# Kernel optimization log

Measured on AMD Instinct MI355X. Metric: run time of the kernel, lower is better.

## Reference

```python
import jax, jax.numpy as jnp
import numpy as np

HIDDEN = 1024
HEADS = 16
HEAD_DIM = HIDDEN // HEADS
EPS = 1e-5


def setup_inputs() -> dict:
    key = jax.random.key(0)
    ks = jax.random.split(key, 9)
    B, S, H = 2, 2048, HIDDEN
    scale = 1.0 / np.sqrt(H)
    inp = {
        "hidden_states": jax.random.normal(ks[0], (B, S, H), dtype=jnp.float32),
        "Wq": jax.random.normal(ks[1], (H, H), dtype=jnp.float32) * scale,
        "bq": jnp.zeros((H,), jnp.float32),
        "Wk": jax.random.normal(ks[2], (H, H), dtype=jnp.float32) * scale,
        "bk": jnp.zeros((H,), jnp.float32),
        "Wv": jax.random.normal(ks[3], (H, H), dtype=jnp.float32) * scale,
        "bv": jnp.zeros((H,), jnp.float32),
        "Wo": jax.random.normal(ks[4], (H, H), dtype=jnp.float32) * scale,
        "bo": jnp.zeros((H,), jnp.float32),
        "gamma": jnp.ones((H,), jnp.float32),
        "beta": jnp.zeros((H,), jnp.float32),
    }
    return inp


def reference(hidden_states, Wq, bq, Wk, bk, Wv, bv, Wo, bo, gamma, beta):
    B, S, H = hidden_states.shape
    residual = hidden_states

    def shape(x):  # [B,S,H] -> [B,heads,S,head_dim]
        return x.reshape(B, S, HEADS, HEAD_DIM).transpose(0, 2, 1, 3)

    q = shape(hidden_states @ Wq + bq)
    k = shape(hidden_states @ Wk + bk)
    v = shape(hidden_states @ Wv + bv)

    scores = jnp.einsum("bhqd,bhkd->bhqk", q, k) / jnp.sqrt(
        jnp.asarray(HEAD_DIM, hidden_states.dtype))
    probs = jax.nn.softmax(scores, axis=-1)
    context = jnp.einsum("bhqk,bhkd->bhqd", probs, v)
    context = context.transpose(0, 2, 1, 3).reshape(B, S, H)

    output = context @ Wo + bo
    x = output + residual
    mu = jnp.mean(x, axis=-1, keepdims=True)
    var = jnp.mean(jnp.square(x - mu), axis=-1, keepdims=True)
    return (x - mu) * jax.lax.rsqrt(var + EPS) * gamma + beta
```

## Files before the change

kernel.cpp:

```cpp
#include <hip/hip_runtime.h>
#include <hip/hip_bf16.h>
#include <math.h>

#define HIDDEN 1024
#define HEADS 16
#define HEAD_DIM 64
#define EPS 1e-5f

typedef __attribute__((ext_vector_type(8))) short bf16x8;
typedef __attribute__((ext_vector_type(4))) float f32x4;

#if defined(__has_builtin)
#if __has_builtin(__builtin_amdgcn_exp2f)
#define EXP2(x) __builtin_amdgcn_exp2f(x)
#endif
#endif
#ifndef EXP2
#define EXP2(x) exp2f(x)
#endif

#define QSCALE 0.18033688011112042f

__device__ __forceinline__ short f2bf(float f) {
    union { float f; unsigned u; } v; v.f = f;
    unsigned r = v.u + 0x7fffu + ((v.u >> 16) & 1u);
    return (short)(r >> 16);
}

__device__ __forceinline__ void gl_lds16(const void* g, void* l) {
    __builtin_amdgcn_global_load_lds(
        (const __attribute__((address_space(1))) void*)g,
        (__attribute__((address_space(3))) void*)l, 16, 0, 0);
}

__global__ __launch_bounds__(256) void prep_kernel(
    const float* __restrict__ X,
    const float* __restrict__ Wq, const float* __restrict__ Wk,
    const float* __restrict__ Wv, const float* __restrict__ Wo,
    const float* __restrict__ bq, const float* __restrict__ bk,
    const float* __restrict__ bv,
    short* __restrict__ Xb, short* __restrict__ Wt3, short* __restrict__ Wot,
    float* __restrict__ b3)
{
    const int z = blockIdx.z;
    __shared__ short tile[32][33];
    if (z < 4) {
        const float* W = (z == 0) ? Wq : (z == 1) ? Wk : (z == 2) ? Wv : Wo;
        short* dst = (z < 3) ? (Wt3 + (size_t)z * 1024 * 1024) : Wot;
        const float scale = (z == 0) ? QSCALE : 1.0f;
        int n0 = blockIdx.x * 32, k0 = blockIdx.y * 32;
        int tx = threadIdx.x & 31, ty = threadIdx.x >> 5;
        #pragma unroll
        for (int i = 0; i < 32; i += 8)
            tile[ty + i][tx] = f2bf(W[(size_t)(k0 + ty + i) * 1024 + n0 + tx] * scale);
        __syncthreads();
        #pragma unroll
        for (int i = 0; i < 32; i += 8)
            dst[(size_t)(n0 + ty + i) * 1024 + k0 + tx] = tile[tx][ty + i];
    } else if (z < 8) {
        int l = (z - 4) * 1024 + blockIdx.y * 32 + blockIdx.x;
        int i = (l * 256 + threadIdx.x) * 4;
        float4 v = *(const float4*)(X + i);
        short o[4] = { f2bf(v.x), f2bf(v.y), f2bf(v.z), f2bf(v.w) };
        *(uint2*)(Xb + i) = *(uint2*)o;
    } else {
        int i = (blockIdx.y * 32 + blockIdx.x) * 256 + threadIdx.x;
        if (i < 3072) {
            float v = (i < 1024) ? bq[i] * QSCALE
                    : (i < 2048) ? bk[i - 1024] : bv[i - 2048];
            b3[i] = v;
        }
    }
}

template<int BM>
__global__ __launch_bounds__(256) void gemm_bt_mfma(
    const short* __restrict__ A, const short* __restrict__ Bt,
    const float* __restrict__ bias,
    void* __restrict__ C0, int ldc0,
    void* __restrict__ C1, int split_col, int ldc1,
    const float* __restrict__ resid,
    int M, int N, int K, int out_bf16)
{
    constexpr int MT = BM / 32;
    constexpr int ACH = BM / 32;
    __shared__ short As[2][BM * 64];
    __shared__ short Bs[2][128 * 64];
    const int tid = threadIdx.x;
    const int wave = tid >> 6, lane = tid & 63;
    const int ln16 = lane & 15, quad = lane >> 4;
    const int wm = (wave >> 1) * (BM / 2), wn = (wave & 1) * 64;

    const int gx = gridDim.x;
    int bid = blockIdx.y * gx + blockIdx.x;
    const int cpx = (gx * gridDim.y) >> 3;
    bid = (bid & 7) * cpx + (bid >> 3);
    const int brow = (bid / gx) * BM, bcol = (bid % gx) * 128;

    const int kr  = lane >> 3;
    const int kb8 = lane & 7;

    f32x4 acc[MT][4];
    #pragma unroll
    for (int mt = 0; mt < MT; ++mt)
        #pragma unroll
        for (int nt = 0; nt < 4; ++nt) acc[mt][nt] = (f32x4){0.f, 0.f, 0.f, 0.f};

    auto stage = [&](int p, int kt) {
        #pragma unroll
        for (int i = 0; i < ACH; ++i) {
            int ci = wave * ACH + i;
            int r  = ci * 8 + kr;
            int csrc = (kb8 ^ (r & 7)) * 8;
            gl_lds16(A + (size_t)(brow + r) * K + kt * 64 + csrc, &As[p][ci * 512]);
        }
        #pragma unroll
        for (int i = 0; i < 4; ++i) {
            int ci = wave * 4 + i;
            int r  = ci * 8 + kr;
            int csrc = (kb8 ^ (r & 7)) * 8;
            gl_lds16(Bt + (size_t)(bcol + r) * K + kt * 64 + csrc, &Bs[p][ci * 512]);
        }
    };

    const int NKT = K / 64;
    stage(0, 0);
    __syncthreads();

    for (int kt = 0; kt < NKT; ++kt) {
        const int cur = kt & 1;
        if (kt + 1 < NKT) stage(cur ^ 1, kt + 1);

        #pragma unroll
        for (int kk = 0; kk < 2; ++kk) {
            bf16x8 af[MT], bf[4];
            #pragma unroll
            for (int mt = 0; mt < MT; ++mt) {
                int r = wm + mt * 16 + ln16;
                af[mt] = *(const bf16x8*)&As[cur][r * 64 + (((kk * 4 + quad) ^ (r & 7)) * 8)];
            }
            #pragma unroll
            for (int nt = 0; nt < 4; ++nt) {
                int r = wn + nt * 16 + ln16;
                bf[nt] = *(const bf16x8*)&Bs[cur][r * 64 + (((kk * 4 + quad) ^ (r & 7)) * 8)];
            }
            #pragma unroll
            for (int mt = 0; mt < MT; ++mt)
                #pragma unroll
                for (int nt = 0; nt < 4; ++nt)
                    acc[mt][nt] = __builtin_amdgcn_mfma_f32_16x16x32_bf16(
                        af[mt], bf[nt], acc[mt][nt], 0, 0, 0);
        }
        __syncthreads();
    }

    void* Cp = C0; int ld = ldc0; int coff = 0;
    if (bcol >= split_col) { Cp = C1; ld = ldc1; coff = split_col; }

    #pragma unroll
    for (int mt = 0; mt < MT; ++mt) {
        #pragma unroll
        for (int r = 0; r < 4; ++r) {
            int row = brow + wm + mt * 16 + quad * 4 + r;
            #pragma unroll
            for (int nt = 0; nt < 4; ++nt) {
                int col = bcol + wn + nt * 16 + ln16;
                float v = acc[mt][nt][r] + bias[col];
                if (resid) v += resid[(size_t)row * N + col];
                if (out_bf16) ((short*)Cp)[(size_t)row * ld + (col - coff)] = f2bf(v);
                else          ((float*)Cp)[(size_t)row * ld + (col - coff)] = v;
            }
        }
    }
}

__global__ __launch_bounds__(256) void vtranspose_kernel(
    const short* __restrict__ Vb, short* __restrict__ VT)
{
    __shared__ short t[64][72];
    const int c0 = blockIdx.x * 64;
    const int r0 = blockIdx.y * 64;
    const int tid = threadIdx.x;
    #pragma unroll
    for (int i = 0; i < 2; ++i) {
        int idx = tid + i * 256;
        int r = idx >> 3, cc = (idx & 7) * 8;
        *(uint4*)&t[r][cc] = *(const uint4*)(Vb + (size_t)(r0 + r) * 1024 + c0 + cc);
    }
    __syncthreads();
    #pragma unroll
    for (int i = 0; i < 2; ++i) {
        int idx = tid + i * 256;
        int c = idx >> 3, rr = (idx & 7) * 8;
        short tmp[8];
        #pragma unroll
        for (int j = 0; j < 8; ++j) tmp[j] = t[rr + j][c];
        *(uint4*)(VT + (size_t)(c0 + c) * 4096 + r0 + rr) = *(uint4*)tmp;
    }
}

__global__ __launch_bounds__(256, 3) void attn_mfma_kernel(
    const short* __restrict__ QKb, const short* __restrict__ VT,
    short* __restrict__ Ctx)
{
    const int S = 2048;
    const int h = blockIdx.x, qt = blockIdx.y, b = blockIdx.z;
    const int tid = threadIdx.x;
    const int wave = tid >> 6, lane = tid & 63;
    const int ln16 = lane & 15, quad = lane >> 4;

    __shared__ alignas(16) char smem[49152];
    short* Ks = (short*)smem;
    short* Vs = (short*)(smem + 16384);
    char*  Pw = smem + 32768 + wave * 4096;

    bf16x8 qf[4][2];
    #pragma unroll
    for (int qg = 0; qg < 4; ++qg)
        #pragma unroll
        for (int kb = 0; kb < 2; ++kb)
            qf[qg][kb] = *(const bf16x8*)(QKb +
                (size_t)(b * S + qt * 64 + qg * 16 + ln16) * 2048 +
                h * 64 + kb * 32 + quad * 8);

    f32x4 of[4][4];
    float rs[4] = {0.f, 0.f, 0.f, 0.f};
    #pragma unroll
    for (int qg = 0; qg < 4; ++qg)
        #pragma unroll
        for (int nt = 0; nt < 4; ++nt) of[qg][nt] = (f32x4){0.f, 0.f, 0.f, 0.f};

    auto stage = [&](int kt) {
        const int kr  = lane >> 3;
        const int kb8 = lane & 7;
        const int vr  = lane >> 4;
        const int vb16 = lane & 15;
        #pragma unroll
        for (int i = 0; i < 4; ++i) {
            int r = wave * 32 + i * 8 + kr;
            int ksrc = (kb8 ^ (r & 7)) * 8;
            gl_lds16(QKb + (size_t)(b * S + kt * 128 + r) * 2048 + 1024 + h * 64 + ksrc,
                     Ks + (wave * 32 + i * 8) * 64);
            int d = wave * 16 + i * 4 + vr;
            int vsrc = (vb16 ^ (d & 15)) * 8;
            gl_lds16(VT + (size_t)(h * 64 + d) * 4096 + b * S + kt * 128 + vsrc,
                     Vs + (wave * 16 + i * 4) * 128);
        }
    };

    stage(0);
    __syncthreads();

    const int t0w = wave * 32;

    for (int kt = 0; kt < 16; ++kt) {
        bf16x8 kf[2][2], vf[4];
        #pragma unroll
        for (int kblk = 0; kblk < 2; ++kblk) {
            int rloc = t0w + kblk * 16 + ln16;
            kf[kblk][0] = *(const bf16x8*)&Ks[rloc * 64 + ((quad ^ (rloc & 7)) * 8)];
            kf[kblk][1] = *(const bf16x8*)&Ks[rloc * 64 + (((4 + quad) ^ (rloc & 7)) * 8)];
        }
        #pragma unroll
        for (int nt = 0; nt < 4; ++nt) {
            int d = nt * 16 + ln16;
            vf[nt] = *(const bf16x8*)&Vs[d * 128 + (((wave * 4 + quad) ^ (d & 15)) * 8)];
        }
        __syncthreads();
        if (kt + 1 < 16) stage(kt + 1);

        #pragma unroll
        for (int kblk = 0; kblk < 2; ++kblk) {
            f32x4 a[4];
            __builtin_amdgcn_s_setprio(1);
            #pragma unroll
            for (int qg = 0; qg < 4; ++qg) {
                a[qg] = (f32x4){0.f, 0.f, 0.f, 0.f};
                a[qg] = __builtin_amdgcn_mfma_f32_16x16x32_bf16(kf[kblk][0], qf[qg][0], a[qg], 0, 0, 0);
            }
            #pragma unroll
            for (int qg = 0; qg < 4; ++qg)
                a[qg] = __builtin_amdgcn_mfma_f32_16x16x32_bf16(kf[kblk][1], qf[qg][1], a[qg], 0, 0, 0);
            __builtin_amdgcn_s_setprio(0);
            #pragma unroll
            for (int qg = 0; qg < 4; ++qg) {
                float p0 = EXP2(a[qg][0]), p1 = EXP2(a[qg][1]);
                float p2 = EXP2(a[qg][2]), p3 = EXP2(a[qg][3]);
                rs[qg] += (p0 + p1) + (p2 + p3);
                union { __hip_bfloat162 h2; unsigned u; } c01, c23;
                c01.h2 = __float22bfloat162_rn(make_float2(p0, p1));
                c23.h2 = __float22bfloat162_rn(make_float2(p2, p3));
                uint2 w; w.x = c01.u; w.y = c23.u;
                int qrow = qg * 16 + ln16;
                int key = (qrow >> 1) & 3;
                int bblk = (kblk * 2 + (quad >> 1)) ^ key;
                *(uint2*)(Pw + qrow * 64 + bblk * 16 + (quad & 1) * 8) = w;
            }
        }

        bf16x8 pf[4];
        #pragma unroll
        for (int qg = 0; qg < 4; ++qg) {
            int qrow = qg * 16 + ln16;
            int key = (qrow >> 1) & 3;
            pf[qg] = *(const bf16x8*)(Pw + qrow * 64 + ((quad ^ key) * 16));
        }
        __builtin_amdgcn_s_setprio(1);
        #pragma unroll
        for (int nt = 0; nt < 4; ++nt)
            #pragma unroll
            for (int qg = 0; qg < 4; ++qg)
                of[qg][nt] = __builtin_amdgcn_mfma_f32_16x16x32_bf16(pf[qg], vf[nt], of[qg][nt], 0, 0, 0);
        __builtin_amdgcn_s_setprio(0);

        __syncthreads();
    }

    #pragma unroll
    for (int qg = 0; qg < 4; ++qg) {
        rs[qg] += __shfl_xor(rs[qg], 16, 64);
        rs[qg] += __shfl_xor(rs[qg], 32, 64);
    }

    float* Rw = (float*)(smem + wave * 4864);
    float* Lb = (float*)(smem + 4 * 4864);

    if (quad == 0) {
        #pragma unroll
        for (int qg = 0; qg < 4; ++qg)
            Lb[wave * 64 + qg * 16 + ln16] = rs[qg];
    }

    const int rq  = tid >> 2;
    const int rd0 = (tid & 3) * 4;
    float inv = 0.f;

    #pragma unroll
    for (int nt = 0; nt < 4; ++nt) {
        #pragma unroll
        for (int qg = 0; qg < 4; ++qg)
            #pragma unroll
            for (int r = 0; r < 4; ++r)
                Rw[(qg * 16 + quad * 4 + r) * 19 + ln16] = of[qg][nt][r];
        __syncthreads();
        if (nt == 0) {
            float l = Lb[rq] + Lb[64 + rq] + Lb[128 + rq] + Lb[192 + rq];
            inv = 1.f / l;
        }
        short o4[4];
        #pragma unroll
        for (int j = 0; j < 4; ++j) {
            int d = rd0 + j;
            float s = 0.f;
            #pragma unroll
            for (int w = 0; w < 4; ++w)
                s += ((const float*)(smem + w * 4864))[rq * 19 + d];
            o4[j] = f2bf(s * inv);
        }
        *(uint2*)(Ctx + (size_t)(b * S + qt * 64 + rq) * 1024 + h * 64 + nt * 16 + rd0) =
            *(uint2*)o4;
        __syncthreads();
    }
}

__global__ __launch_bounds__(256) void resln_kernel(
    const float* __restrict__ xin, const float* __restrict__ gamma,
    const float* __restrict__ beta, float* __restrict__ out)
{
    const int row = blockIdx.x;
    const int tid = threadIdx.x;
    const int wid = tid >> 6, lane = tid & 63;
    __shared__ float red[8];

    float4 x = *(const float4*)(xin + (size_t)row * HIDDEN + tid * 4);
    float s = x.x + x.y + x.z + x.w;
    #pragma unroll
    for (int off = 32; off > 0; off >>= 1) s += __shfl_xor(s, off, 64);
    if (lane == 0) red[wid] = s;
    __syncthreads();
    float mu = (red[0] + red[1] + red[2] + red[3]) * (1.f / HIDDEN);

    float dx = x.x - mu, dy = x.y - mu, dz = x.z - mu, dw = x.w - mu;
    float v = dx * dx + dy * dy + dz * dz + dw * dw;
    #pragma unroll
    for (int off = 32; off > 0; off >>= 1) v += __shfl_xor(v, off, 64);
    if (lane == 0) red[4 + wid] = v;
    __syncthreads();
    float var = (red[4] + red[5] + red[6] + red[7]) * (1.f / HIDDEN);
    float rstd = rsqrtf(var + EPS);

    float4 g = *(const float4*)(gamma + tid * 4);
    float4 bt = *(const float4*)(beta + tid * 4);
    float4 o;
    o.x = dx * rstd * g.x + bt.x;
    o.y = dy * rstd * g.y + bt.y;
    o.z = dz * rstd * g.z + bt.z;
    o.w = dw * rstd * g.w + bt.w;
    *(float4*)(out + (size_t)row * HIDDEN + tid * 4) = o;
}

extern "C" void kernel_launch(void* const* d_in, const int* in_sizes, int n_in,
                              void* d_out, int out_size, void* d_ws, size_t ws_size,
                              hipStream_t stream)
{
    const float* X     = (const float*)d_in[0];
    const float* Wq    = (const float*)d_in[1];
    const float* bq    = (const float*)d_in[2];
    const float* Wk    = (const float*)d_in[3];
    const float* bk    = (const float*)d_in[4];
    const float* Wv    = (const float*)d_in[5];
    const float* bv    = (const float*)d_in[6];
    const float* Wo    = (const float*)d_in[7];
    const float* bo    = (const float*)d_in[8];
    const float* gamma = (const float*)d_in[9];
    const float* beta  = (const float*)d_in[10];
    float* out = (float*)d_out;

    const int B = 2, S = 2048;
    const int M = B * S;
    const size_t mat = (size_t)M * HIDDEN;
    (void)mat;

    char* ws = (char*)d_ws;
    short* Xb  = (short*)(ws);
    short* VT  = (short*)(ws);
    short* Wot = (short*)(ws + (8ull << 20));
    short* Wt3 = (short*)(ws + (10ull << 20));
    float* b3  = (float*)(ws + (16ull << 20));
    short* QKb = (short*)(ws + (17ull << 20));
    float* Pj  = (float*)(ws + (17ull << 20));
    short* Vb  = (short*)(ws + (33ull << 20));
    short* Ctx = (short*)(ws + (33ull << 20));

    dim3 blk(256);

    prep_kernel<<<dim3(32, 32, 9), blk, 0, stream>>>(
        X, Wq, Wk, Wv, Wo, bq, bk, bv, Xb, Wt3, Wot, b3);

    dim3 qkvgrid(3072 / 128, M / 128);
    gemm_bt_mfma<128><<<qkvgrid, blk, 0, stream>>>(Xb, Wt3, b3,
                                              QKb, 2048, Vb, 2048, 1024,
                                              nullptr, M, 3072, HIDDEN, 1);

    vtranspose_kernel<<<dim3(16, 64), blk, 0, stream>>>(Vb, VT);

    dim3 agrid(HEADS, S / 64, B);
    attn_mfma_kernel<<<agrid, blk, 0, stream>>>(QKb, VT, Ctx);

    dim3 ogrid(HIDDEN / 128, M / 64);
    gemm_bt_mfma<64><<<ogrid, blk, 0, stream>>>(Ctx, Wot, bo,
                                            Pj, 1024, nullptr, 1 << 30, 0,
                                            X, M, HIDDEN, HIDDEN, 0);

    resln_kernel<<<M, blk, 0, stream>>>(Pj, gamma, beta, out);
}
```

Before: 260.6 us.

## Fuse V transpose into QKV GEMM epilogue and double-buffer attention K/V tiles

The QKV GEMM now writes the V columns directly in transposed layout, so the separate vtranspose kernel and its extra round trip through memory go away. Both the GEMM and attention loops drop the trailing __syncthreads and instead wait on vmcnt plus a barrier at the top of each iteration. The attention kernel double-buffers its K/V tiles in a larger shared-memory allocation and loads V fragments just in time, which lowers occupancy from 3 to 2 blocks per CU. The transposed epilogue issues narrow 8-byte strided stores that may coalesce poorly.

```diff
diff --git a/kernel.cpp b/kernel.cpp
--- a/kernel.cpp
+++ b/kernel.cpp
@@ -78,7 +78,7 @@
     const short* __restrict__ A, const short* __restrict__ Bt,
     const float* __restrict__ bias,
     void* __restrict__ C0, int ldc0,
-    void* __restrict__ C1, int split_col, int ldc1,
+    void* __restrict__ C1, int split_col, int ldc1, int c1_trans,
     const float* __restrict__ resid,
     int M, int N, int K, int out_bf16)
 {
@@ -125,10 +125,12 @@
 
     const int NKT = K / 64;
     stage(0, 0);
-    __syncthreads();
 
     for (int kt = 0; kt < NKT; ++kt) {
         const int cur = kt & 1;
+        asm volatile("s_waitcnt vmcnt(0)" ::: "memory");
+        __builtin_amdgcn_s_barrier();
+        __builtin_amdgcn_sched_barrier(0);
         if (kt + 1 < NKT) stage(cur ^ 1, kt + 1);
 
         #pragma unroll
@@ -151,7 +153,24 @@
                     acc[mt][nt] = __builtin_amdgcn_mfma_f32_16x16x32_bf16(
                         af[mt], bf[nt], acc[mt][nt], 0, 0, 0);
         }
-        __syncthreads();
+    }
+
+    if (bcol >= split_col && c1_trans) {
+        #pragma unroll
+        for (int mt = 0; mt < MT; ++mt) {
+            int row0 = brow + wm + mt * 16 + quad * 4;
+            #pragma unroll
+            for (int nt = 0; nt < 4; ++nt) {
+                int col = bcol + wn + nt * 16 + ln16;
+                float bv = bias[col];
+                short o4[4];
+                #pragma unroll
+                for (int r = 0; r < 4; ++r) o4[r] = f2bf(acc[mt][nt][r] + bv);
+                *(uint2*)((short*)C1 + (size_t)(col - split_col) * ldc1 + row0) =
+                    *(uint2*)o4;
+            }
+        }
+        return;
     }
 
     void* Cp = C0; int ld = ldc0; int coff = 0;
@@ -174,32 +193,7 @@
     }
 }
 
-__global__ __launch_bounds__(256) void vtranspose_kernel(
-    const short* __restrict__ Vb, short* __restrict__ VT)
-{
-    __shared__ short t[64][72];
-    const int c0 = blockIdx.x * 64;
-    const int r0 = blockIdx.y * 64;
-    const int tid = threadIdx.x;
-    #pragma unroll
-    for (int i = 0; i < 2; ++i) {
-        int idx = tid + i * 256;
-        int r = idx >> 3, cc = (idx & 7) * 8;
-        *(uint4*)&t[r][cc] = *(const uint4*)(Vb + (size_t)(r0 + r) * 1024 + c0 + cc);
-    }
-    __syncthreads();
-    #pragma unroll
-    for (int i = 0; i < 2; ++i) {
-        int idx = tid + i * 256;
-        int c = idx >> 3, rr = (idx & 7) * 8;
-        short tmp[8];
-        #pragma unroll
-        for (int j = 0; j < 8; ++j) tmp[j] = t[rr + j][c];
-        *(uint4*)(VT + (size_t)(c0 + c) * 4096 + r0 + rr) = *(uint4*)tmp;
-    }
-}
-
-__global__ __launch_bounds__(256, 3) void attn_mfma_kernel(
+__global__ __launch_bounds__(256, 2) void attn_mfma_kernel(
     const short* __restrict__ QKb, const short* __restrict__ VT,
     short* __restrict__ Ctx)
 {
@@ -209,10 +203,8 @@
     const int wave = tid >> 6, lane = tid & 63;
     const int ln16 = lane & 15, quad = lane >> 4;
 
-    __shared__ alignas(16) char smem[49152];
-    short* Ks = (short*)smem;
-    short* Vs = (short*)(smem + 16384);
-    char*  Pw = smem + 32768 + wave * 4096;
+    __shared__ alignas(16) char smem[81920];
+    char* Pw = smem + 65536 + wave * 4096;
 
     bf16x8 qf[4][2];
     #pragma unroll
@@ -230,7 +222,9 @@
         #pragma unroll
         for (int nt = 0; nt < 4; ++nt) of[qg][nt] = (f32x4){0.f, 0.f, 0.f, 0.f};
 
-    auto stage = [&](int kt) {
+    auto stage = [&](int p, int kt) {
+        short* ksb = (short*)(smem + p * 16384);
+        short* vsb = (short*)(smem + 32768 + p * 16384);
         const int kr  = lane >> 3;
         const int kb8 = lane & 7;
         const int vr  = lane >> 4;
@@ -240,52 +234,42 @@
             int r = wave * 32 + i * 8 + kr;
             int ksrc = (kb8 ^ (r & 7)) * 8;
             gl_lds16(QKb + (size_t)(b * S + kt * 128 + r) * 2048 + 1024 + h * 64 + ksrc,
-                     Ks + (wave * 32 + i * 8) * 64);
+                     ksb + (wave * 32 + i * 8) * 64);
             int d = wave * 16 + i * 4 + vr;
             int vsrc = (vb16 ^ (d & 15)) * 8;
             gl_lds16(VT + (size_t)(h * 64 + d) * 4096 + b * S + kt * 128 + vsrc,
-                     Vs + (wave * 16 + i * 4) * 128);
+                     vsb + (wave * 16 + i * 4) * 128);
         }
     };
 
-    stage(0);
-    __syncthreads();
+    stage(0, 0);
 
     const int t0w = wave * 32;
 
     for (int kt = 0; kt < 16; ++kt) {
-        bf16x8 kf[2][2], vf[4];
+        const int cur = kt & 1;
+        asm volatile("s_waitcnt vmcnt(0)" ::: "memory");
+        __builtin_amdgcn_s_barrier();
+        __builtin_amdgcn_sched_barrier(0);
+        if (kt + 1 < 16) stage(cur ^ 1, kt + 1);
+
+        const short* ks = (const short*)(smem + cur * 16384);
+        const short* vs = (const short*)(smem + 32768 + cur * 16384);
+
         #pragma unroll
         for (int kblk = 0; kblk < 2; ++kblk) {
             int rloc = t0w + kblk * 16 + ln16;
-            kf[kblk][0] = *(const bf16x8*)&Ks[rloc * 64 + ((quad ^ (rloc & 7)) * 8)];
-            kf[kblk][1] = *(const bf16x8*)&Ks[rloc * 64 + (((4 + quad) ^ (rloc & 7)) * 8)];
-        }
-        #pragma unroll
-        for (int nt = 0; nt < 4; ++nt) {
-            int d = nt * 16 + ln16;
-            vf[nt] = *(const bf16x8*)&Vs[d * 128 + (((wave * 4 + quad) ^ (d & 15)) * 8)];
-        }
-        __syncthreads();
-        if (kt + 1 < 16) stage(kt + 1);
-
-        #pragma unroll
-        for (int kblk = 0; kblk < 2; ++kblk) {
-            f32x4 a[4];
-            __builtin_amdgcn_s_setprio(1);
+            bf16x8 kf0 = *(const bf16x8*)&ks[rloc * 64 + ((quad ^ (rloc & 7)) * 8)];
+            bf16x8 kf1 = *(const bf16x8*)&ks[rloc * 64 + (((4 + quad) ^ (rloc & 7)) * 8)];
             #pragma unroll
             for (int qg = 0; qg < 4; ++qg) {
-                a[qg] = (f32x4){0.f, 0.f, 0.f, 0.f};
-                a[qg] = __builtin_amdgcn_mfma_f32_16x16x32_bf16(kf[kblk][0], qf[qg][0], a[qg], 0, 0, 0);
-            }
-            #pragma unroll
-            for (int qg = 0; qg < 4; ++qg)
-                a[qg] = __builtin_amdgcn_mfma_f32_16x16x32_bf16(kf[kblk][1], qf[qg][1], a[qg], 0, 0, 0);
-            __builtin_amdgcn_s_setprio(0);
-            #pragma unroll
-            for (int qg = 0; qg < 4; ++qg) {
-                float p0 = EXP2(a[qg][0]), p1 = EXP2(a[qg][1]);
-                float p2 = EXP2(a[qg][2]), p3 = EXP2(a[qg][3]);
+                f32x4 a = (f32x4){0.f, 0.f, 0.f, 0.f};
+                __builtin_amdgcn_s_setprio(1);
+                a = __builtin_amdgcn_mfma_f32_16x16x32_bf16(kf0, qf[qg][0], a, 0, 0, 0);
+                a = __builtin_amdgcn_mfma_f32_16x16x32_bf16(kf1, qf[qg][1], a, 0, 0, 0);
+                __builtin_amdgcn_s_setprio(0);
+                float p0 = EXP2(a[0]), p1 = EXP2(a[1]);
+                float p2 = EXP2(a[2]), p3 = EXP2(a[3]);
                 rs[qg] += (p0 + p1) + (p2 + p3);
                 union { __hip_bfloat162 h2; unsigned u; } c01, c23;
                 c01.h2 = __float22bfloat162_rn(make_float2(p0, p1));
@@ -307,14 +291,17 @@
         }
         __builtin_amdgcn_s_setprio(1);
         #pragma unroll
-        for (int nt = 0; nt < 4; ++nt)
+        for (int nt = 0; nt < 4; ++nt) {
+            int d = nt * 16 + ln16;
+            bf16x8 vf = *(const bf16x8*)&vs[d * 128 + (((wave * 4 + quad) ^ (d & 15)) * 8)];
             #pragma unroll
             for (int qg = 0; qg < 4; ++qg)
-                of[qg][nt] = __builtin_amdgcn_mfma_f32_16x16x32_bf16(pf[qg], vf[nt], of[qg][nt], 0, 0, 0);
+                of[qg][nt] = __builtin_amdgcn_mfma_f32_16x16x32_bf16(pf[qg], vf, of[qg][nt], 0, 0, 0);
+        }
         __builtin_amdgcn_s_setprio(0);
-
-        __syncthreads();
-    }
+    }
+
+    __syncthreads();
 
     #pragma unroll
     for (int qg = 0; qg < 4; ++qg) {
@@ -418,19 +405,16 @@
 
     const int B = 2, S = 2048;
     const int M = B * S;
-    const size_t mat = (size_t)M * HIDDEN;
-    (void)mat;
 
     char* ws = (char*)d_ws;
     short* Xb  = (short*)(ws);
-    short* VT  = (short*)(ws);
+    short* Ctx = (short*)(ws);
     short* Wot = (short*)(ws + (8ull << 20));
     short* Wt3 = (short*)(ws + (10ull << 20));
     float* b3  = (float*)(ws + (16ull << 20));
     short* QKb = (short*)(ws + (17ull << 20));
     float* Pj  = (float*)(ws + (17ull << 20));
-    short* Vb  = (short*)(ws + (33ull << 20));
-    short* Ctx = (short*)(ws + (33ull << 20));
+    short* VT  = (short*)(ws + (33ull << 20));
 
     dim3 blk(256);
 
@@ -439,17 +423,15 @@
 
     dim3 qkvgrid(3072 / 128, M / 128);
     gemm_bt_mfma<128><<<qkvgrid, blk, 0, stream>>>(Xb, Wt3, b3,
-                                              QKb, 2048, Vb, 2048, 1024,
+                                              QKb, 2048, VT, 2048, 4096, 1,
                                               nullptr, M, 3072, HIDDEN, 1);
-
-    vtranspose_kernel<<<dim3(16, 64), blk, 0, stream>>>(Vb, VT);
 
     dim3 agrid(HEADS, S / 64, B);
     attn_mfma_kernel<<<agrid, blk, 0, stream>>>(QKb, VT, Ctx);
 
     dim3 ogrid(HIDDEN / 128, M / 64);
     gemm_bt_mfma<64><<<ogrid, blk, 0, stream>>>(Ctx, Wot, bo,
-                                            Pj, 1024, nullptr, 1 << 30, 0,
+                                            Pj, 1024, nullptr, 1 << 30, 0, 0,
                                             X, M, HIDDEN, HIDDEN, 0);
 
     resln_kernel<<<M, blk, 0, stream>>>(Pj, gamma, beta, out);
```

Result: faster. 227.1 us (-12.9%).
